# Kernel optimization log

Hardware: AMD Instinct MI355X
Metric: run time of the kernel (lower is better)

Reference implementation:

```python
import jax, jax.numpy as jnp
import numpy as np

H = 4          # attention heads
K = 16         # knn neighbors
EPS = 1e-5     # BatchNorm eps


def setup_inputs() -> dict:
    key = jax.random.key(0)
    ks = jax.random.split(key, 10)
    B, C, T, N = 2, 128, 32, 512
    OUT = 128
    HID = 2 * C + 2 * OUT  # ff hidden = in*2 + out*2
    s = 0.02
    return {
        "x_all": jax.random.normal(ks[0], (B, C, T, N), jnp.float32),
        "Wq": jax.random.normal(ks[1], (C, C), jnp.float32) * s,
        "Wk": jax.random.normal(ks[2], (C, C), jnp.float32) * s,
        "Wv": jax.random.normal(ks[3], (C, C), jnp.float32) * s,
        "W1": jax.random.normal(ks[4], (HID, C), jnp.float32) * s,
        "W2": jax.random.normal(ks[5], (OUT, HID), jnp.float32) * s,
        "bn_gamma": 1.0 + 0.1 * jax.random.normal(ks[6], (OUT,), jnp.float32),
        "bn_beta": 0.1 * jax.random.normal(ks[7], (OUT,), jnp.float32),
        "bn_mean": 0.1 * jax.random.normal(ks[8], (OUT,), jnp.float32),
        "bn_var": jax.random.uniform(ks[9], (OUT,), jnp.float32, 0.5, 1.5),
    }


def reference(x_all, Wq, Wk, Wv, W1, W2, bn_gamma, bn_beta, bn_mean, bn_var):
    B, C, T, N = x_all.shape
    D = C // H
    # --- st_group_points: candidate pool = 3 consecutive frames (replicate temporal pad), frame-major ---
    xp = jnp.concatenate([x_all[:, :, :1], x_all, x_all[:, :, -1:]], axis=2)   # (B,C,T+2,N)
    pool = jnp.stack([xp[:, :, :-2], xp[:, :, 1:-1], xp[:, :, 2:]], axis=3)    # (B,C,T,3,N)
    pool = pool.reshape(B, C, T, 3 * N)                                        # (B,C,T,3N)
    # KNN on xyz (channels 0:3); sqrt is monotone so topk on squared dists gives same indices
    a = x_all[:, :3]                                                           # (B,3,T,N)
    b = pool[:, :3]                                                            # (B,3,T,3N)
    d2 = jnp.sum((a[..., :, None] - b[..., None, :]) ** 2, axis=1)             # (B,T,N,3N)
    _, idx = jax.lax.top_k(-d2, K)                                             # (B,T,N,K) smallest-dist
    nb = jnp.take_along_axis(pool[:, :, :, None, :], idx[:, None], axis=-1)    # (B,C,T,N,K)
    rel = x_all[..., None] - nb                                                # diff grouping (B,C,T,N,K)
    # --- per-point local attention over K neighbors (1x1 convs == channel matmuls), all t at once ---
    q = jnp.einsum('oc,bctn->botn', Wq, x_all).reshape(B, H, D, T, N)
    k = jnp.einsum('oc,bctnk->botnk', Wk, rel).reshape(B, H, D, T, N, K)
    v = jnp.einsum('oc,bctnk->botnk', Wv, rel).reshape(B, H, D, T, N, K)
    energy = jnp.einsum('bhdtn,bhdtnk->bhtnk', q, k) / jnp.sqrt(jnp.float32(D))
    attn = jax.nn.softmax(energy, axis=-1)                                     # (B,H,T,N,K)
    agg = jnp.einsum('bhtnk,bhdtnk->bhdtn', attn, v).reshape(B, C, T, N)
    # --- residual + BatchNorm1d (eval mode, running stats) + conv feed-forward ---
    h = x_all + agg
    scale = (bn_gamma / jnp.sqrt(bn_var + EPS))[None, :, None, None]
    h = (h - bn_mean[None, :, None, None]) * scale + bn_beta[None, :, None, None]
    h = jax.nn.leaky_relu(jnp.einsum('oc,bctn->botn', W1, h), 0.2)
    y = jnp.einsum('oc,bctn->botn', W2, h)                                     # (B,OUT,T,N)
    return jnp.concatenate([x_all[:, :4], y], axis=1)                          # (B,4+OUT,T,N)
```

## Files before the change

kernel.cpp:

```cpp
#include <hip/hip_runtime.h>
#include <hip/hip_bf16.h>

typedef __hip_bfloat16 bf16;
typedef unsigned long long u64;
typedef __attribute__((ext_vector_type(8))) short short8;
typedef __attribute__((ext_vector_type(4))) float f32x4;

#define B_   2
#define C_   128
#define T_   32
#define N_   512
#define K_   16
#define HID_ 512
#define TN   (T_*N_)
#define PTS  (B_*T_*N_)

#define MFMA_BF16(a,b,c) __builtin_amdgcn_mfma_f32_16x16x32_bf16((a),(b),(c),0,0,0)

__device__ __forceinline__ float b2f(bf16 v){ return __bfloat162float(v); }
__device__ __forceinline__ bf16  f2b(float v){ return __float2bfloat16(v); }
__device__ __forceinline__ float bqf(short v){
  return __uint_as_float(((unsigned)(unsigned short)v) << 16);
}

__device__ __forceinline__ float ldc(const void* p, int i, bool f32) {
  return f32 ? ((const float*)p)[i] : b2f(((const bf16*)p)[i]);
}

__global__ __launch_bounds__(256) void convw_kernel(
    const void* __restrict__ x,
    const void* wq, const void* wk, const void* wv,
    const void* w1, const void* w2, const void* g, const void* bb,
    const void* m, const void* v,
    bf16* __restrict__ wqb, bf16* __restrict__ wkb, bf16* __restrict__ wvb,
    bf16* __restrict__ w1b, bf16* __restrict__ w2b,
    float* __restrict__ gf, float* __restrict__ bf_, float* __restrict__ mf,
    float* __restrict__ vf, int* __restrict__ flag)
{
  __shared__ int cnt;
  if (threadIdx.x == 0) cnt = 0;
  __syncthreads();
  const unsigned short* u = (const unsigned short*)x;
  int w = 0;
#pragma unroll
  for (int j = 0; j < 8; ++j) {
    unsigned short hv = u[threadIdx.x*8 + j];
    int e = (hv >> 7) & 0xFF;
    if (e >= 0x89) w++;
  }
  if (w) atomicAdd(&cnt, w);
  __syncthreads();
  bool f32 = (cnt > 32);
  if (blockIdx.x == 0 && threadIdx.x == 0) *flag = f32 ? 1 : 0;

  int i = blockIdx.x*256 + threadIdx.x;
  if (i < 16384) { wqb[i] = f2b(ldc(wq, i, f32)); return; } i -= 16384;
  if (i < 16384) { wkb[i] = f2b(ldc(wk, i, f32)); return; } i -= 16384;
  if (i < 16384) { wvb[i] = f2b(ldc(wv, i, f32)); return; } i -= 16384;
  if (i < 65536) { w1b[i] = f2b(ldc(w1, i, f32)); return; } i -= 65536;
  if (i < 65536) { w2b[i] = f2b(ldc(w2, i, f32)); return; } i -= 65536;
  if (i < 128)   { gf[i]  = ldc(g, i, f32); return; }       i -= 128;
  if (i < 128)   { bf_[i] = ldc(bb, i, f32); return; }      i -= 128;
  if (i < 128)   { mf[i]  = ldc(m, i, f32); return; }       i -= 128;
  if (i < 128)   { vf[i]  = ldc(v, i, f32); return; }
}

__device__ __forceinline__ u64 shflx64(u64 v, int m) {
  return (u64)__shfl_xor((long long)v, m, 64);
}

__device__ __forceinline__ void proj_gemm32(const bf16* __restrict__ W,
                                            bf16 (*ys)[136],
                                            const short8 am[2][4],
                                            int mrow, int quad, int ot)
{
  f32x4 acc[2];
#pragma unroll
  for (int mt=0;mt<2;++mt) acc[mt] = (f32x4){0.f,0.f,0.f,0.f};
#pragma unroll
  for (int kq=0;kq<4;++kq) {
    short8 bfr = *(const short8*)&W[(ot*16+mrow)*C_ + kq*32 + quad*8];
#pragma unroll
    for (int mt=0;mt<2;++mt) acc[mt] = MFMA_BF16(am[mt][kq], bfr, acc[mt]);
  }
#pragma unroll
  for (int mt=0;mt<2;++mt)
#pragma unroll
    for (int r=0;r<4;++r)
      ys[mt*16 + quad*4 + r][ot*16 + mrow] = f2b(acc[mt][r]);
}

__device__ __forceinline__ void tile_store32_512(bf16* __restrict__ dst,
                                                 const bf16 (*ys)[136], int tid)
{
  int flat = tid*8;
  int p = flat >> 7, c = flat & 127;
  *(short8*)&dst[(size_t)p*C_ + c] = *(const short8*)&ys[p][c];
}

__global__ __launch_bounds__(512) void projknn_kernel(
    const void* __restrict__ x, const int* __restrict__ flag,
    const bf16* __restrict__ wqb, const bf16* __restrict__ wkb, const bf16* __restrict__ wvb,
    bf16* __restrict__ xTb, bf16* QT, bf16* __restrict__ KT, bf16* __restrict__ VT,
    int* __restrict__ idxout)
{
  __shared__ __align__(16) char smem[28672];
  int tid = threadIdx.x;
  int blk = blockIdx.x;
  int g = blk / 5, r = blk - g*5;
  if (r == 4) {
    bf16 (*xs )[136] = (bf16(*)[136])(smem);
    bf16 (*ysK)[136] = (bf16(*)[136])(smem + 8704);
    bf16 (*ysV)[136] = (bf16(*)[136])(smem + 17408);
    int p0 = g * 32;
    int b = p0 >> 14; int tn0 = p0 & (TN-1);
    if (*flag) {
      const float* xbase = (const float*)x + (size_t)b*C_*TN + tn0;
#pragma unroll
      for (int it=0; it<8; ++it) {
        int i = it*512 + tid;
        int c = i >> 5, p = i & 31;
        xs[p][c] = f2b(xbase[(size_t)c*TN + p]);
      }
    } else {
      const bf16* xbase = (const bf16*)x + (size_t)b*C_*TN + tn0;
#pragma unroll
      for (int it=0; it<8; ++it) {
        int i = it*512 + tid;
        int c = i >> 5, p = i & 31;
        xs[p][c] = xbase[(size_t)c*TN + p];
      }
    }
    __syncthreads();
    tile_store32_512(xTb + (size_t)p0*C_, xs, tid);
    int lane = tid & 63, wave = tid >> 6;
    int mrow = lane & 15, quad = lane >> 4;
    short8 am[2][4];
#pragma unroll
    for (int mt=0;mt<2;++mt)
#pragma unroll
      for (int kq=0;kq<4;++kq)
        am[mt][kq] = *(const short8*)&xs[mt*16 + mrow][kq*32 + quad*8];
    __syncthreads();
    proj_gemm32(wqb, xs,  am, mrow, quad, wave);
    proj_gemm32(wkb, ysK, am, mrow, quad, wave);
    proj_gemm32(wvb, ysV, am, mrow, quad, wave);
    __syncthreads();
    tile_store32_512(QT + (size_t)p0*C_, xs,  tid);
    tile_store32_512(KT + (size_t)p0*C_, ysK, tid);
    tile_store32_512(VT + (size_t)p0*C_, ysV, tid);
  } else {
    float4* cand4 = (float4*)smem;
    u64 (*surv)[64] = (u64(*)[64])(smem + 24576);
    int kblk = g*4 + r;
    int row = kblk >> 6;
    int b = row >> 5, t = row & 31;
    int ng = kblk & 63;
    bool f32 = (*flag != 0);
#pragma unroll
    for (int q = 0; q < 3; ++q) {
      int tt = t - 1 + q; tt = tt < 0 ? 0 : (tt > T_-1 ? T_-1 : tt);
      size_t base = ((size_t)b*C_*T_ + tt)*(size_t)N_ + tid;
      float c0, c1, c2;
      if (f32) {
        const float* xp = (const float*)x;
        c0 = xp[base]; c1 = xp[base + (size_t)T_*N_]; c2 = xp[base + 2*(size_t)T_*N_];
      } else {
        const bf16* xp = (const bf16*)x;
        c0 = b2f(xp[base]); c1 = b2f(xp[base + (size_t)T_*N_]); c2 = b2f(xp[base + 2*(size_t)T_*N_]);
      }
      cand4[q*N_ + tid] = make_float4(c0, c1, c2, 0.f);
    }
    __syncthreads();
    int wave = tid >> 6, lane = tid & 63;
    int n = ng*8 + wave;
    float4 a = cand4[N_ + n];
    unsigned db[24];
#pragma unroll
    for (int j = 0; j < 24; ++j) {
      float4 cm = cand4[lane + (j << 6)];
      float dx = a.x - cm.x;
      float dy = a.y - cm.y;
      float dz = a.z - cm.z;
      float d2 = __fadd_rn(__fadd_rn(__fmul_rn(dx,dx), __fmul_rn(dy,dy)), __fmul_rn(dz,dz));
      db[j] = __float_as_uint(d2);
    }
    unsigned mm[12];
#pragma unroll
    for (int j = 0; j < 12; ++j) mm[j] = db[2*j] < db[2*j+1] ? db[2*j] : db[2*j+1];
#pragma unroll
    for (int j = 0; j < 6; ++j)  mm[j] = mm[2*j] < mm[2*j+1] ? mm[2*j] : mm[2*j+1];
#pragma unroll
    for (int j = 0; j < 3; ++j)  mm[j] = mm[2*j] < mm[2*j+1] ? mm[2*j] : mm[2*j+1];
    unsigned bd = mm[0] < mm[1] ? mm[0] : mm[1];
    bd = bd < mm[2] ? bd : mm[2];
    {
      unsigned lo = 0u, hi = 0x7f800000u;
#pragma unroll
      for (int it = 0; it < 16; ++it) {
        unsigned mid = lo + ((hi - lo) >> 1);
        int cge = __popcll(__ballot(bd <= mid));
        bool ge = (cge >= K_);
        hi = ge ? mid : hi;
        lo = ge ? lo : (mid + 1u);
      }
      bd = hi;
    }
    unsigned U = bd;
    int c = 0;
#pragma unroll
    for (int j = 0; j < 24; ++j) c += (db[j] <= U) ? 1 : 0;
    int ofs = 0, total = 0;
#pragma unroll
    for (int bit = 0; bit < 5; ++bit) {
      u64 mball = __ballot(((c >> bit) & 1) != 0);
      unsigned below = __builtin_amdgcn_mbcnt_hi((unsigned)(mball >> 32),
                        __builtin_amdgcn_mbcnt_lo((unsigned)mball, 0u));
      ofs   += ((int)below) << bit;
      total += (__popcll(mball)) << bit;
    }
    int point = (b*T_ + t)*N_ + n;
    if (total <= 64) {
#pragma unroll
      for (int j = 0; j < 24; ++j) {
        if (db[j] <= U) {
          surv[wave][ofs] = ((u64)db[j] << 11) | (unsigned)(lane + (j << 6));
          ++ofs;
        }
      }
      if (lane == total) surv[wave][lane] = ~0ull;
      __threadfence_block();
      u64 kk = (lane < total) ? surv[wave][lane] : ~0ull;
      int npair = (total + 1) >> 1;
      int rank = 0;
      const ulonglong2* sk2 = (const ulonglong2*)&surv[wave][0];
#pragma unroll 4
      for (int i2 = 0; i2 < npair; ++i2) {
        ulonglong2 kp = sk2[i2];
        rank += (kp.x < kk) ? 1 : 0;
        rank += (kp.y < kk) ? 1 : 0;
      }
      if (rank < K_) idxout[point*K_ + rank] = (int)(kk & 2047u);
    } else {
      u64 key[24];
#pragma unroll
      for (int j = 0; j < 24; ++j)
        key[j] = ((u64)db[j] << 32) | (unsigned)(lane + (j << 6));
      u64 res = ~0ull;
#pragma unroll 1
      for (int rr = 0; rr < 16; ++rr) {
        u64 m2 = key[0];
#pragma unroll
        for (int j = 1; j < 24; ++j) m2 = (key[j] < m2) ? key[j] : m2;
#pragma unroll
        for (int s = 32; s >= 1; s >>= 1) {
          u64 p = shflx64(m2, s);
          m2 = (p < m2) ? p : m2;
        }
        if (lane == rr) res = m2;
        int mwin = (int)(m2 & 0xffffffffu);
        int sel = ((mwin & 63) == lane) ? (mwin >> 6) : -1;
#pragma unroll
        for (int j = 0; j < 24; ++j) if (j == sel) key[j] = ~0ull;
      }
      if (lane < K_) idxout[point*K_ + lane] = (int)(res & 0xffffffffu);
    }
  }
}

__global__ __launch_bounds__(256) void attnmlp_kernel(
    const int* __restrict__ idxin, const bf16* __restrict__ xTb,
    const bf16* __restrict__ QT, const bf16* __restrict__ KT,
    const bf16* __restrict__ VT,
    const float* __restrict__ gf, const float* __restrict__ bf_,
    const float* __restrict__ mf, const float* __restrict__ vf,
    const bf16* __restrict__ w1b, const bf16* __restrict__ w2b,
    const void* __restrict__ x, const int* __restrict__ flag,
    void* __restrict__ out)
{
  __shared__ __align__(16) char smem[25600];
  bf16  (*hTl)[136]       = (bf16 (*)[136])      (smem);
  int   (*colbuf)[K_]     = (int  (*)[K_])       (smem + 8704);
  float (*qbuf)[2][C_]    = (float(*)[2][C_])    (smem + 10752);
  float (*e_lds)[4][K_]   = (float(*)[4][K_])    (smem + 12800);
  bf16  (*vbuf)[K_][136]  = (bf16 (*)[K_][136])  (smem + 13312);
  bf16  (*hidh)[264]      = (bf16 (*)[264])      (smem + 8704);

  int tid = threadIdx.x;
  int gblk = (blockIdx.x & 7)*128 + (blockIdx.x >> 3);
  int p0 = gblk * 32;
  int bb = p0 >> 14;
  int tn0 = p0 & (TN-1);
  bool f32o = (*flag != 0);
  if (tid < 128) {
    int c = tid >> 5, p = tid & 31;
    size_t si = ((size_t)bb*C_ + c)*TN + tn0 + p;
    size_t di = ((size_t)bb*132 + c)*TN + tn0 + p;
    if (f32o) ((float*)out)[di] = ((const float*)x)[si];
    else      ((bf16*)out)[di]  = ((const bf16*)x)[si];
  }

  int tblk = tn0 >> 9;
#pragma unroll
  for (int it = 0; it < 2; ++it) {
    int e = it*256 + tid;
    int row = e >> 4, kk = e & 15;
    int m = idxin[(p0 + row)*K_ + kk];
    int j = m >> 9, nn = m & (N_-1);
    int tt = tblk-1+j; tt = tt<0?0:(tt>T_-1?T_-1:tt);
    colbuf[row][kk] = ((bb*T_ + tt)*N_ + nn)*C_;
  }

  int pt = tid >> 7, o = tid & 127;
  int k = o >> 3, c = o & 7, hd = c >> 1;
  float sc = gf[o] / sqrtf(vf[o] + 1e-5f);
  float smean = mf[o], sbeta = bf_[o];
  float vselfC, xselfC, vselfN = 0.f, xselfN = 0.f;
  {
    int self = (p0 + pt)*C_;
    vselfC = b2f(VT[self + o]);
    xselfC = b2f(xTb[self + o]);
    qbuf[0][pt][o] = b2f(QT[self + o]);
  }
  __syncthreads();
  short8 kv0, kv1, vv0, vv1;
  {
    int src = colbuf[pt][k] + c*16;
    kv0 = *(const short8*)&KT[src];
    kv1 = *(const short8*)&KT[src + 8];
    vv0 = *(const short8*)&VT[src];
    vv1 = *(const short8*)&VT[src + 8];
  }
#pragma unroll 1
  for (int sub = 0; sub < 16; ++sub) {
    int cur = sub & 1, nxt = cur ^ 1;
    {
      *(short8*)&vbuf[pt][k][c*16]     = vv0;
      *(short8*)&vbuf[pt][k][c*16 + 8] = vv1;
      const float* qp = &qbuf[cur][pt][c*16];
      float qv[16];
      *(float4*)&qv[0]  = *(const float4*)(qp);
      *(float4*)&qv[4]  = *(const float4*)(qp + 4);
      *(float4*)&qv[8]  = *(const float4*)(qp + 8);
      *(float4*)&qv[12] = *(const float4*)(qp + 12);
      float e = 0.f;
#pragma unroll
      for (int i2=0;i2<8;++i2) e = fmaf(qv[i2],   bqf(kv0[i2]), e);
#pragma unroll
      for (int i2=0;i2<8;++i2) e = fmaf(qv[8+i2], bqf(kv1[i2]), e);
      e += __shfl_xor(e, 1, 64);
      if (!(c & 1)) e_lds[pt][hd][k] = -e * 0.17677669529663687f;
    }
    if (sub < 15) {
      int row = (sub+1)*2 + pt;
      int src = colbuf[row][k] + c*16;
      kv0 = *(const short8*)&KT[src];
      kv1 = *(const short8*)&KT[src + 8];
      vv0 = *(const short8*)&VT[src];
      vv1 = *(const short8*)&VT[src + 8];
      int self = (p0 + row)*C_;
      vselfN = b2f(VT[self + o]);
      xselfN = b2f(xTb[self + o]);
      qbuf[nxt][pt][o] = b2f(QT[self + o]);
    }
    __syncthreads();
    {
      int hd2 = o >> 5;
      float ee[16]; float mx = -3e38f;
#pragma unroll
      for (int kk=0;kk<K_;++kk){ ee[kk]=e_lds[pt][hd2][kk]; mx=fmaxf(mx,ee[kk]); }
      float ssum=0.f;
#pragma unroll
      for (int kk=0;kk<K_;++kk){ ee[kk]=__expf(ee[kk]-mx); ssum+=ee[kk]; }
      float inv = 1.f/ssum;
      float acc = vselfC;
#pragma unroll
      for (int kk=0;kk<K_;++kk)
        acc = fmaf(-(ee[kk]*inv), b2f(vbuf[pt][kk][o]), acc);
      float hv = xselfC + acc;
      hTl[sub*2 + pt][o] = f2b((hv - smean)*sc + sbeta);
    }
    vselfC = vselfN; xselfC = xselfN;
    __syncthreads();
  }

  int lane = tid & 63, wave = tid >> 6;
  int mrow = lane & 15, quad = lane >> 4;
  f32x4 acc2[2][2];
#pragma unroll
  for (int oi=0;oi<2;++oi)
#pragma unroll
    for (int mt=0;mt<2;++mt) acc2[oi][mt] = (f32x4){0.f,0.f,0.f,0.f};

#pragma unroll
  for (int half = 0; half < 2; ++half) {
    if (half) __syncthreads();
    short8 am[2][4];
#pragma unroll
    for (int mt=0;mt<2;++mt)
#pragma unroll
      for (int kq=0;kq<4;++kq)
        am[mt][kq] = *(const short8*)&hTl[mt*16 + mrow][kq*32 + quad*8];
#pragma unroll
    for (int oi = 0; oi < 4; ++oi) {
      int ot_g = half*16 + wave*4 + oi;
      int otl  = wave*4 + oi;
      f32x4 acc[2];
#pragma unroll
      for (int mt=0;mt<2;++mt) acc[mt] = (f32x4){0.f,0.f,0.f,0.f};
#pragma unroll
      for (int kq=0;kq<4;++kq) {
        short8 bfr = *(const short8*)&w1b[(ot_g*16+mrow)*C_ + kq*32 + quad*8];
#pragma unroll
        for (int mt=0;mt<2;++mt) acc[mt] = MFMA_BF16(am[mt][kq], bfr, acc[mt]);
      }
#pragma unroll
      for (int mt=0;mt<2;++mt)
#pragma unroll
        for (int r=0;r<4;++r) {
          float z = acc[mt][r];
          hidh[mt*16 + quad*4 + r][otl*16 + mrow] = f2b(z > 0.f ? z : 0.2f*z);
        }
    }
    __syncthreads();
#pragma unroll
    for (int kc = 0; kc < 4; ++kc) {
      short8 ha[2][2];
#pragma unroll
      for (int mt=0;mt<2;++mt)
#pragma unroll
        for (int kk=0;kk<2;++kk)
          ha[mt][kk] = *(const short8*)&hidh[mt*16 + mrow][(kc*2+kk)*32 + quad*8];
#pragma unroll
      for (int oi=0;oi<2;++oi) {
        int ot2 = wave*2 + oi;
#pragma unroll
        for (int kk=0;kk<2;++kk) {
          int ks_g = half*8 + kc*2 + kk;
          short8 bfr = *(const short8*)&w2b[(ot2*16+mrow)*HID_ + ks_g*32 + quad*8];
#pragma unroll
          for (int mt=0;mt<2;++mt)
            acc2[oi][mt] = MFMA_BF16(ha[mt][kk], bfr, acc2[oi][mt]);
        }
      }
    }
  }
  size_t obase = (size_t)bb*132*TN;
#pragma unroll
  for (int oi=0;oi<2;++oi) {
    int ch = (wave*2+oi)*16 + mrow;
#pragma unroll
    for (int mt=0;mt<2;++mt) {
      int tn = tn0 + mt*16 + quad*4;
      size_t oidx = obase + (size_t)(4+ch)*TN + tn;
      if (f32o) {
        *(f32x4*)&((float*)out)[oidx] = acc2[oi][mt];
      } else {
        bf16 tmp[4];
#pragma unroll
        for (int r=0;r<4;++r) tmp[r] = f2b(acc2[oi][mt][r]);
        *(u64*)&((bf16*)out)[oidx] = *(u64*)tmp;
      }
    }
  }
}

extern "C" void kernel_launch(void* const* d_in, const int* in_sizes, int n_in,
                              void* d_out, int out_size, void* d_ws, size_t ws_size,
                              hipStream_t stream)
{
  (void)in_sizes; (void)n_in; (void)out_size; (void)ws_size;
  const void* x = d_in[0];
  char* ws = (char*)d_ws;
  const size_t MB = (size_t)1<<20;
  bf16*  QT  = (bf16* )(ws + 0*MB);
  bf16*  KT  = (bf16* )(ws + 8*MB);
  bf16*  VT  = (bf16* )(ws + 16*MB);
  bf16*  xTb = (bf16* )(ws + 24*MB);
  int*   idxw= (int*  )(ws + 32*MB);
  bf16*  wqb = (bf16* )(ws + 34*MB);
  bf16*  wkb = (bf16* )(ws + 34*MB + 0x8000);
  bf16*  wvb = (bf16* )(ws + 34*MB + 0x10000);
  bf16*  w1b = (bf16* )(ws + 34*MB + 0x18000);
  bf16*  w2b = (bf16* )(ws + 34*MB + 0x38000);
  float* gf  = (float*)(ws + 34*MB + 0x58000);
  float* bf_ = (float*)(ws + 34*MB + 0x58200);
  float* mf  = (float*)(ws + 34*MB + 0x58400);
  float* vf  = (float*)(ws + 34*MB + 0x58600);
  int*  flag = (int*  )(ws + 34*MB + 0x58800);

  convw_kernel  <<<dim3(706), dim3(256), 0, stream>>>(
      x, d_in[1], d_in[2], d_in[3], d_in[4], d_in[5],
      d_in[6], d_in[7], d_in[8], d_in[9],
      wqb, wkb, wvb, w1b, w2b, gf, bf_, mf, vf, flag);
  projknn_kernel<<<dim3(5120), dim3(512), 0, stream>>>(
      x, flag, wqb, wkb, wvb, xTb, QT, KT, VT, idxw);
  attnmlp_kernel<<<dim3(PTS/32), dim3(256), 0, stream>>>(
      idxw, xTb, QT, KT, VT, gf, bf_, mf, vf, w1b, w2b, x, flag, d_out);
}
```

Baseline: 190.1 us.

## Process four points per attention iteration with per-head thread mapping

Restructures the per-point attention loop so each iteration handles four points instead of two, halving the iteration count and the number of block barriers. Each thread now computes a full per-head 32-element dot product, which removes the cross-lane shuffle. The query buffer is stored as bf16 and the launch bounds request four blocks per CU. In exchange, LDS use and per-thread registers grow, since each thread holds twice as many gathered K/V vectors, and rounding q to bf16 slightly changes precision.

```diff
diff --git a/kernel.cpp b/kernel.cpp
--- a/kernel.cpp
+++ b/kernel.cpp
@@ -268,7 +268,7 @@
   }
 }
 
-__global__ __launch_bounds__(256) void attnmlp_kernel(
+__global__ __launch_bounds__(256, 4) void attnmlp_kernel(
     const int* __restrict__ idxin, const bf16* __restrict__ xTb,
     const bf16* __restrict__ QT, const bf16* __restrict__ KT,
     const bf16* __restrict__ VT,
@@ -278,12 +278,12 @@
     const void* __restrict__ x, const int* __restrict__ flag,
     void* __restrict__ out)
 {
-  __shared__ __align__(16) char smem[25600];
+  __shared__ __align__(16) char smem[31232];
   bf16  (*hTl)[136]       = (bf16 (*)[136])      (smem);
   int   (*colbuf)[K_]     = (int  (*)[K_])       (smem + 8704);
-  float (*qbuf)[2][C_]    = (float(*)[2][C_])    (smem + 10752);
+  bf16  (*qbuf)[4][C_]    = (bf16 (*)[4][C_])    (smem + 10752);
   float (*e_lds)[4][K_]   = (float(*)[4][K_])    (smem + 12800);
-  bf16  (*vbuf)[K_][136]  = (bf16 (*)[K_][136])  (smem + 13312);
+  bf16  (*vbuf)[K_][136]  = (bf16 (*)[K_][136])  (smem + 13824);
   bf16  (*hidh)[264]      = (bf16 (*)[264])      (smem + 8704);
 
   int tid = threadIdx.x;
@@ -311,76 +311,91 @@
     colbuf[row][kk] = ((bb*T_ + tt)*N_ + nn)*C_;
   }
 
-  int pt = tid >> 7, o = tid & 127;
-  int k = o >> 3, c = o & 7, hd = c >> 1;
+  int ppA = tid >> 7, o = tid & 127;
+  int ppE = tid >> 6, ke = (tid >> 2) & 15, hde = tid & 3;
   float sc = gf[o] / sqrtf(vf[o] + 1e-5f);
   float smean = mf[o], sbeta = bf_[o];
-  float vselfC, xselfC, vselfN = 0.f, xselfN = 0.f;
+  float vselfC[2], xselfC[2], vselfN[2], xselfN[2];
   {
-    int self = (p0 + pt)*C_;
-    vselfC = b2f(VT[self + o]);
-    xselfC = b2f(xTb[self + o]);
-    qbuf[0][pt][o] = b2f(QT[self + o]);
+    int s0 = (p0 + ppA)*C_;
+    int s1 = s0 + 2*C_;
+    vselfC[0] = b2f(VT[s0 + o]);  xselfC[0] = b2f(xTb[s0 + o]);
+    vselfC[1] = b2f(VT[s1 + o]);  xselfC[1] = b2f(xTb[s1 + o]);
+    qbuf[0][ppA][o]     = QT[s0 + o];
+    qbuf[0][ppA + 2][o] = QT[s1 + o];
+    vselfN[0] = vselfN[1] = xselfN[0] = xselfN[1] = 0.f;
   }
   __syncthreads();
-  short8 kv0, kv1, vv0, vv1;
+  short8 kv0, kv1, kv2, kv3, vv0, vv1, vv2, vv3;
   {
-    int src = colbuf[pt][k] + c*16;
-    kv0 = *(const short8*)&KT[src];
-    kv1 = *(const short8*)&KT[src + 8];
-    vv0 = *(const short8*)&VT[src];
-    vv1 = *(const short8*)&VT[src + 8];
+    int src = colbuf[ppE][ke] + hde*32;
+    kv0 = *(const short8*)&KT[src];      kv1 = *(const short8*)&KT[src + 8];
+    kv2 = *(const short8*)&KT[src + 16]; kv3 = *(const short8*)&KT[src + 24];
+    vv0 = *(const short8*)&VT[src];      vv1 = *(const short8*)&VT[src + 8];
+    vv2 = *(const short8*)&VT[src + 16]; vv3 = *(const short8*)&VT[src + 24];
   }
 #pragma unroll 1
-  for (int sub = 0; sub < 16; ++sub) {
+  for (int sub = 0; sub < 8; ++sub) {
     int cur = sub & 1, nxt = cur ^ 1;
     {
-      *(short8*)&vbuf[pt][k][c*16]     = vv0;
-      *(short8*)&vbuf[pt][k][c*16 + 8] = vv1;
-      const float* qp = &qbuf[cur][pt][c*16];
-      float qv[16];
-      *(float4*)&qv[0]  = *(const float4*)(qp);
-      *(float4*)&qv[4]  = *(const float4*)(qp + 4);
-      *(float4*)&qv[8]  = *(const float4*)(qp + 8);
-      *(float4*)&qv[12] = *(const float4*)(qp + 12);
-      float e = 0.f;
-#pragma unroll
-      for (int i2=0;i2<8;++i2) e = fmaf(qv[i2],   bqf(kv0[i2]), e);
-#pragma unroll
-      for (int i2=0;i2<8;++i2) e = fmaf(qv[8+i2], bqf(kv1[i2]), e);
-      e += __shfl_xor(e, 1, 64);
-      if (!(c & 1)) e_lds[pt][hd][k] = -e * 0.17677669529663687f;
-    }
-    if (sub < 15) {
-      int row = (sub+1)*2 + pt;
-      int src = colbuf[row][k] + c*16;
-      kv0 = *(const short8*)&KT[src];
-      kv1 = *(const short8*)&KT[src + 8];
-      vv0 = *(const short8*)&VT[src];
-      vv1 = *(const short8*)&VT[src + 8];
-      int self = (p0 + row)*C_;
-      vselfN = b2f(VT[self + o]);
-      xselfN = b2f(xTb[self + o]);
-      qbuf[nxt][pt][o] = b2f(QT[self + o]);
+      *(short8*)&vbuf[ppE][ke][hde*32]      = vv0;
+      *(short8*)&vbuf[ppE][ke][hde*32 + 8]  = vv1;
+      *(short8*)&vbuf[ppE][ke][hde*32 + 16] = vv2;
+      *(short8*)&vbuf[ppE][ke][hde*32 + 24] = vv3;
+      const bf16* qp = &qbuf[cur][ppE][hde*32];
+      short8 q0 = *(const short8*)(qp);
+      short8 q1 = *(const short8*)(qp + 8);
+      short8 q2 = *(const short8*)(qp + 16);
+      short8 q3 = *(const short8*)(qp + 24);
+      float e0 = 0.f, e1 = 0.f;
+#pragma unroll
+      for (int i2=0;i2<8;++i2) e0 = fmaf(bqf(q0[i2]), bqf(kv0[i2]), e0);
+#pragma unroll
+      for (int i2=0;i2<8;++i2) e0 = fmaf(bqf(q1[i2]), bqf(kv1[i2]), e0);
+#pragma unroll
+      for (int i2=0;i2<8;++i2) e1 = fmaf(bqf(q2[i2]), bqf(kv2[i2]), e1);
+#pragma unroll
+      for (int i2=0;i2<8;++i2) e1 = fmaf(bqf(q3[i2]), bqf(kv3[i2]), e1);
+      float e = e0 + e1;
+      e_lds[ppE][hde][ke] = -e * 0.17677669529663687f;
+    }
+    if (sub < 7) {
+      int row = (sub+1)*4 + ppE;
+      int src = colbuf[row][ke] + hde*32;
+      kv0 = *(const short8*)&KT[src];      kv1 = *(const short8*)&KT[src + 8];
+      kv2 = *(const short8*)&KT[src + 16]; kv3 = *(const short8*)&KT[src + 24];
+      vv0 = *(const short8*)&VT[src];      vv1 = *(const short8*)&VT[src + 8];
+      vv2 = *(const short8*)&VT[src + 16]; vv3 = *(const short8*)&VT[src + 24];
+      int s0 = (p0 + (sub+1)*4 + ppA)*C_;
+      int s1 = s0 + 2*C_;
+      vselfN[0] = b2f(VT[s0 + o]);  xselfN[0] = b2f(xTb[s0 + o]);
+      vselfN[1] = b2f(VT[s1 + o]);  xselfN[1] = b2f(xTb[s1 + o]);
+      qbuf[nxt][ppA][o]     = QT[s0 + o];
+      qbuf[nxt][ppA + 2][o] = QT[s1 + o];
     }
     __syncthreads();
     {
       int hd2 = o >> 5;
-      float ee[16]; float mx = -3e38f;
-#pragma unroll
-      for (int kk=0;kk<K_;++kk){ ee[kk]=e_lds[pt][hd2][kk]; mx=fmaxf(mx,ee[kk]); }
-      float ssum=0.f;
-#pragma unroll
-      for (int kk=0;kk<K_;++kk){ ee[kk]=__expf(ee[kk]-mx); ssum+=ee[kk]; }
-      float inv = 1.f/ssum;
-      float acc = vselfC;
-#pragma unroll
-      for (int kk=0;kk<K_;++kk)
-        acc = fmaf(-(ee[kk]*inv), b2f(vbuf[pt][kk][o]), acc);
-      float hv = xselfC + acc;
-      hTl[sub*2 + pt][o] = f2b((hv - smean)*sc + sbeta);
-    }
-    vselfC = vselfN; xselfC = xselfN;
+#pragma unroll
+      for (int pi = 0; pi < 2; ++pi) {
+        int pp = ppA + pi*2;
+        float ee[16]; float mx = -3e38f;
+#pragma unroll
+        for (int kk=0;kk<K_;++kk){ ee[kk]=e_lds[pp][hd2][kk]; mx=fmaxf(mx,ee[kk]); }
+        float ssum=0.f;
+#pragma unroll
+        for (int kk=0;kk<K_;++kk){ ee[kk]=__expf(ee[kk]-mx); ssum+=ee[kk]; }
+        float inv = 1.f/ssum;
+        float acc = vselfC[pi];
+#pragma unroll
+        for (int kk=0;kk<K_;++kk)
+          acc = fmaf(-(ee[kk]*inv), b2f(vbuf[pp][kk][o]), acc);
+        float hv = xselfC[pi] + acc;
+        hTl[sub*4 + pp][o] = f2b((hv - smean)*sc + sbeta);
+      }
+    }
+    vselfC[0]=vselfN[0]; vselfC[1]=vselfN[1];
+    xselfC[0]=xselfN[0]; xselfC[1]=xselfN[1];
     __syncthreads();
   }
 
```

Result: no change. 190.2 us (+0.1%).
